# Performance work log

Hardware: AMD Instinct MI355X
Metric: run time of the kernel (lower is better)

Reference implementation:

```python
import jax, jax.numpy as jnp
import numpy as np

N_NODES = 100000
N_EDGES = 1600000
D_IN = 128
D_OUT = 128
BN_EPS = 1e-5


def setup_inputs() -> dict:
    key = jax.random.key(0)
    k1, k2, k3 = jax.random.split(key, 3)
    x = jax.random.normal(k1, (N_NODES, D_IN), dtype=jnp.float32)
    edge_index = jax.random.randint(k2, (2, N_EDGES), 0, N_NODES, dtype=jnp.int64)
    glorot = float(np.sqrt(6.0 / (D_IN + D_OUT)))
    W = jax.random.uniform(k3, (D_IN, D_OUT), dtype=jnp.float32, minval=-glorot, maxval=glorot)
    b = jnp.zeros((D_OUT,), dtype=jnp.float32)
    gamma = jnp.ones((D_OUT,), dtype=jnp.float32)
    beta = jnp.zeros((D_OUT,), dtype=jnp.float32)
    return {"x": x, "edge_index": edge_index, "W": W, "b": b, "gamma": gamma, "beta": beta}


def reference(x, edge_index, W, b, gamma, beta):
    N = x.shape[0]
    # Linear transform first (as in GCNConv.forward): [N, D_out]
    h = x @ W
    row, col = edge_index[0], edge_index[1]
    # remove_self_loops equivalent: zero out weights of self-loop edges (static shape)
    ew = (row != col).astype(h.dtype)
    loop = jnp.arange(N, dtype=edge_index.dtype)
    row_a = jnp.concatenate([row, loop])
    col_a = jnp.concatenate([col, loop])
    ew_a = jnp.concatenate([ew, jnp.ones((N,), h.dtype)])  # add_self_loops fill=1.0
    # D^{-1/2} A D^{-1/2}: degree over source (row) indices, as in GCNConv.norm
    deg = jax.ops.segment_sum(ew_a, row_a, num_segments=N)
    safe = jnp.where(deg > 0, deg, 1.0)
    deg_inv_sqrt = jnp.where(deg > 0, 1.0 / jnp.sqrt(safe), 0.0)
    norm = deg_inv_sqrt[row_a] * ew_a * deg_inv_sqrt[col_a]
    # message: norm * x_j (gather source), aggregate 'add' at target (col)
    msg = norm[:, None] * h[row_a]
    out = jax.ops.segment_sum(msg, col_a, num_segments=N) + b
    # activation
    out = jax.nn.relu(out)
    # BatchNorm1d (training mode: batch statistics, biased variance)
    mean = out.mean(axis=0)
    var = ((out - mean) ** 2).mean(axis=0)
    out = (out - mean) / jnp.sqrt(var + BN_EPS) * gamma + beta
    return out
```

## Files before the change

kernel.cpp:

```cpp
#include <hip/hip_runtime.h>
#include <math.h>

#define NN 100000
#define NE 1600000
#define D 128
#define BN_EPS 1e-5f
#define NCHUNK 391
#define GSZ4 25000
#define NCH 64
#define CH 25000
#define HW8 6250
#define HSTR 12500

typedef __attribute__((ext_vector_type(8))) short short8;
typedef __attribute__((ext_vector_type(4))) float f32x4;
typedef __attribute__((ext_vector_type(2))) float f32x2;


__device__ __forceinline__ unsigned bf_rne(float f) {
    unsigned u = __float_as_uint(f);
    return (u + 0x7fffu + ((u >> 16) & 1u)) >> 16;
}
__device__ __forceinline__ unsigned pk2(float lo, float hi) {
    return bf_rne(lo) | (bf_rne(hi) << 16);
}

__global__ __launch_bounds__(1024) void k_hist(const int* __restrict__ ei,
                                               unsigned* __restrict__ hist) {
    __shared__ unsigned loc[HSTR];
    const int g = blockIdx.x & 3;
    const int t = blockIdx.x >> 2;
    const int lo = g * GSZ4, hi = lo + GSZ4;
    for (int j = threadIdx.x; j < HSTR; j += 1024) loc[j] = 0u;
    __syncthreads();
    const int end = t * CH + CH;
    for (int i = t * CH + threadIdx.x; i < end; i += 1024) {
        int r = __builtin_nontemporal_load(ei + i);
        int c = __builtin_nontemporal_load(ei + NE + i);
        if (r != c) {
            if (c >= lo && c < hi) {
                int q = c - lo;
                atomicAdd(&loc[q >> 2], 1u << ((q & 3) << 3));
            }
            if (r >= lo && r < hi) {
                int q = r - lo;
                atomicAdd(&loc[HW8 + (q >> 2)], 1u << ((q & 3) << 3));
            }
        }
    }
    __syncthreads();
    unsigned* dst = hist + (unsigned)(g * NCH + t) * HSTR;
    for (int j = threadIdx.x; j < HSTR; j += 1024) dst[j] = loc[j];
}

__global__ void k_cvt(const float* __restrict__ x, unsigned* __restrict__ xh) {
    int i = blockIdx.x * blockDim.x + threadIdx.x;
    if (i < NN * 64) {
        f32x2 v = __builtin_nontemporal_load((const f32x2*)x + i);
        xh[i] = pk2(v.x, v.y);
    }
}

__global__ __launch_bounds__(256) void k_reduce(unsigned* __restrict__ hist,
                                                unsigned* __restrict__ cnt,
                                                float* __restrict__ dinv,
                                                const float* __restrict__ W,
                                                unsigned short* __restrict__ Wht) {
    int id = blockIdx.x * 256 + threadIdx.x;
    if (id < 4 * HW8) {
        int g = id / HW8;
        int w = id - g * HW8;
        unsigned base = (unsigned)(g * NCH) * HSTR + w;
        unsigned r0 = 0, r1 = 0, r2 = 0, r3 = 0;
        unsigned s0 = 0, s1 = 0, s2 = 0, s3 = 0;
        for (int t = 0; t < NCH; ++t) {
            unsigned idx = base + (unsigned)t * HSTR;
            unsigned v = hist[idx];
            hist[idx] = r0 | (r1 << 8) | (r2 << 16) | (r3 << 24);
            r0 += v & 255u; r1 += (v >> 8) & 255u;
            r2 += (v >> 16) & 255u; r3 += v >> 24;
            unsigned d = hist[idx + HW8];
            s0 += d & 255u; s1 += (d >> 8) & 255u;
            s2 += (d >> 16) & 255u; s3 += d >> 24;
        }
        int n0 = g * GSZ4 + 4 * w;
        cnt[n0]     = r0; cnt[n0 + 1] = r1; cnt[n0 + 2] = r2; cnt[n0 + 3] = r3;
        dinv[n0]     = rsqrtf((float)(s0 + 1u));
        dinv[n0 + 1] = rsqrtf((float)(s1 + 1u));
        dinv[n0 + 2] = rsqrtf((float)(s2 + 1u));
        dinv[n0 + 3] = rsqrtf((float)(s3 + 1u));
    } else {
        int i = id - 4 * HW8;
        if (i < D * D) {
            int k = i >> 7, c = i & 127;
            Wht[c * D + k] = (unsigned short)bf_rne(W[i]);
        }
    }
}

__global__ __launch_bounds__(256) void k_scan1(const unsigned* __restrict__ cnt,
                                               unsigned* __restrict__ part) {
    __shared__ unsigned s[256];
    int i = blockIdx.x * 256 + threadIdx.x;
    unsigned v = (i < NN) ? cnt[i] : 0u;
    s[threadIdx.x] = v;
    __syncthreads();
    for (int o = 128; o > 0; o >>= 1) {
        if (threadIdx.x < o) s[threadIdx.x] += s[threadIdx.x + o];
        __syncthreads();
    }
    if (threadIdx.x == 0) part[blockIdx.x] = s[0];
}

__global__ __launch_bounds__(512) void k_scan2(unsigned* __restrict__ part,
                                               float* __restrict__ sums8) {
    __shared__ unsigned s[512];
    int t = threadIdx.x;
    for (int j = t; j < 2048; j += 512) sums8[j] = 0.f;
    unsigned v = (t < NCHUNK) ? part[t] : 0u;
    s[t] = v;
    __syncthreads();
    for (int o = 1; o < 512; o <<= 1) {
        unsigned add = (t >= o) ? s[t - o] : 0u;
        __syncthreads();
        s[t] += add;
        __syncthreads();
    }
    if (t < NCHUNK) part[t] = s[t] - v;
}

__global__ __launch_bounds__(256) void k_scan3(const unsigned* __restrict__ cnt,
                                               const unsigned* __restrict__ part,
                                               unsigned* __restrict__ off) {
    __shared__ unsigned s[256];
    int i = blockIdx.x * 256 + threadIdx.x;
    int t = threadIdx.x;
    unsigned v = (i < NN) ? cnt[i] : 0u;
    s[t] = v;
    __syncthreads();
    for (int o = 1; o < 256; o <<= 1) {
        unsigned add = (t >= o) ? s[t - o] : 0u;
        __syncthreads();
        s[t] += add;
        __syncthreads();
    }
    if (i < NN) off[i] = part[blockIdx.x] + s[t] - v;
}

__global__ __launch_bounds__(1024) void k_scatter(const int* __restrict__ ei,
                                                  const unsigned* __restrict__ off,
                                                  const unsigned* __restrict__ hist,
                                                  int* __restrict__ esrc) {
    __shared__ unsigned curs[GSZ4 / 2];
    const int g = blockIdx.x & 3;
    const int t = blockIdx.x >> 2;
    const int lo = g * GSZ4, hi = lo + GSZ4;
    const unsigned* hb = hist + (unsigned)(g * NCH + t) * HSTR;
    for (int j = threadIdx.x; j < GSZ4 / 2; j += 1024) {
        unsigned hv = hb[j >> 1];
        unsigned sh = (j & 1) << 4;
        unsigned p0 = (hv >> sh) & 255u;
        unsigned p1 = (hv >> (sh + 8)) & 255u;
        curs[j] = p0 | (p1 << 16);
    }
    __syncthreads();
    const int end = t * CH + CH;
    for (int i = t * CH + threadIdx.x; i < end; i += 1024) {
        int r = __builtin_nontemporal_load(ei + i);
        int c = __builtin_nontemporal_load(ei + NE + i);
        if (r == c || c < lo || c >= hi) continue;
        int q = c - lo;
        unsigned sh = (q & 1) << 4;
        unsigned old = atomicAdd(&curs[q >> 1], 1u << sh);
        unsigned pos = off[c] + ((old >> sh) & 0xffffu);
        esrc[pos] = r;
    }
}

__global__ __launch_bounds__(256) void k_gather(const unsigned* __restrict__ xh,
                                                const float* __restrict__ dinv,
                                                const unsigned* __restrict__ off,
                                                const unsigned* __restrict__ cnt,
                                                const int* __restrict__ esrc,
                                                float* __restrict__ out) {
    const int lane = threadIdx.x & 63;
    const int wave = threadIdx.x >> 6;
    const int c = blockIdx.x * 4 + wave;
    if (c >= NN) return;

    const float dc = dinv[c];
    unsigned xc = xh[c * 64 + lane];
    float al = dc * __uint_as_float(xc << 16);
    float ah = dc * __uint_as_float(xc & 0xffff0000u);

    const int base = off[c];
    const int n = cnt[c];
    int i = 0;
    for (; i + 8 <= n; i += 8) {
        int   sv[8];
        float wv[8];
        unsigned pv[8];
        #pragma unroll
        for (int j = 0; j < 8; ++j) sv[j] = esrc[base + i + j];
        #pragma unroll
        for (int j = 0; j < 8; ++j) wv[j] = dinv[sv[j]];
        #pragma unroll
        for (int j = 0; j < 8; ++j) pv[j] = xh[sv[j] * 64 + lane];
        #pragma unroll
        for (int j = 0; j < 8; ++j) {
            al = fmaf(wv[j], __uint_as_float(pv[j] << 16), al);
            ah = fmaf(wv[j], __uint_as_float(pv[j] & 0xffff0000u), ah);
        }
    }
    for (; i + 4 <= n; i += 4) {
        int s0 = esrc[base + i], s1 = esrc[base + i + 1];
        int s2 = esrc[base + i + 2], s3 = esrc[base + i + 3];
        float w0 = dinv[s0], w1 = dinv[s1], w2 = dinv[s2], w3 = dinv[s3];
        unsigned p0 = xh[s0 * 64 + lane], p1 = xh[s1 * 64 + lane];
        unsigned p2 = xh[s2 * 64 + lane], p3 = xh[s3 * 64 + lane];
        al = fmaf(w0, __uint_as_float(p0 << 16), al);
        ah = fmaf(w0, __uint_as_float(p0 & 0xffff0000u), ah);
        al = fmaf(w1, __uint_as_float(p1 << 16), al);
        ah = fmaf(w1, __uint_as_float(p1 & 0xffff0000u), ah);
        al = fmaf(w2, __uint_as_float(p2 << 16), al);
        ah = fmaf(w2, __uint_as_float(p2 & 0xffff0000u), ah);
        al = fmaf(w3, __uint_as_float(p3 << 16), al);
        ah = fmaf(w3, __uint_as_float(p3 & 0xffff0000u), ah);
    }
    for (; i < n; ++i) {
        int s0 = esrc[base + i];
        float w0 = dinv[s0];
        unsigned p0 = xh[s0 * 64 + lane];
        al = fmaf(w0, __uint_as_float(p0 << 16), al);
        ah = fmaf(w0, __uint_as_float(p0 & 0xffff0000u), ah);
    }
    al *= dc;
    ah *= dc;
    *(float2*)&out[c * D + 2 * lane] = make_float2(al, ah);
}

__global__ __launch_bounds__(256, 1) void k_gemm(const float* __restrict__ out,
                                                 unsigned short* __restrict__ rh,
                                                 const unsigned short* __restrict__ Wht,
                                                 const float* __restrict__ b,
                                                 float* __restrict__ sums8) {
    __shared__ float sums_lds[256];
    const int lane = threadIdx.x & 63;
    const int wv = threadIdx.x >> 6;
    const int l15 = lane & 15, l4 = lane >> 4;

    if (threadIdx.x < 256) sums_lds[threadIdx.x] = 0.f;
    __syncthreads();

    short8 bfr[8][4];
    #pragma unroll
    for (int n = 0; n < 8; ++n)
        #pragma unroll
        for (int kk = 0; kk < 4; ++kk)
            bfr[n][kk] = *(const short8*)(Wht + (n * 16 + l15) * D + kk * 32 + l4 * 8);

    float bias8[8];
    #pragma unroll
    for (int n = 0; n < 8; ++n) bias8[n] = b[n * 16 + l15];

    float sl[8], s2l[8];
    #pragma unroll
    for (int n = 0; n < 8; ++n) { sl[n] = 0.f; s2l[n] = 0.f; }

    const int gw = blockIdx.x * 4 + wv;
    #pragma unroll
    for (int t = 0; t < 2; ++t) {
        const int tile = gw * 2 + t;
        if (tile < NN / 16) {
            const int row0 = tile * 16;
            short8 af[4];
            #pragma unroll
            for (int kk = 0; kk < 4; ++kk) {
                const float* ar = out + (row0 + l15) * D + kk * 32 + l4 * 8;
                float4 a0 = *(const float4*)ar;
                float4 a1 = *(const float4*)(ar + 4);
                union { short8 s; unsigned u[4]; } cv;
                cv.u[0] = pk2(a0.x, a0.y);
                cv.u[1] = pk2(a0.z, a0.w);
                cv.u[2] = pk2(a1.x, a1.y);
                cv.u[3] = pk2(a1.z, a1.w);
                af[kk] = cv.s;
            }
            f32x4 acc[8];
            #pragma unroll
            for (int n = 0; n < 8; ++n) acc[n] = (f32x4){0.f, 0.f, 0.f, 0.f};
            #pragma unroll
            for (int n = 0; n < 8; ++n)
                #pragma unroll
                for (int kk = 0; kk < 4; ++kk)
                    acc[n] = __builtin_amdgcn_mfma_f32_16x16x32_bf16(af[kk], bfr[n][kk],
                                                                     acc[n], 0, 0, 0);
            #pragma unroll
            for (int n = 0; n < 8; ++n)
                #pragma unroll
                for (int j = 0; j < 4; ++j) {
                    int row = row0 + l4 * 4 + j;
                    float v = fmaxf(acc[n][j] + bias8[n], 0.f);
                    rh[row * D + n * 16 + l15] = (unsigned short)bf_rne(v);
                    sl[n] += v;
                    s2l[n] = fmaf(v, v, s2l[n]);
                }
        }
    }

    #pragma unroll
    for (int n = 0; n < 8; ++n) {
        float a = sl[n], q = s2l[n];
        a += __shfl_xor(a, 16); a += __shfl_xor(a, 32);
        q += __shfl_xor(q, 16); q += __shfl_xor(q, 32);
        if (l4 == 0) {
            atomicAdd(&sums_lds[n * 16 + l15], a);
            atomicAdd(&sums_lds[128 + n * 16 + l15], q);
        }
    }
    __syncthreads();
    if (threadIdx.x < 256)
        unsafeAtomicAdd(&sums8[(blockIdx.x & 7) * 256 + threadIdx.x],
                        sums_lds[threadIdx.x]);
}

__global__ __launch_bounds__(256) void k_apply(const unsigned* __restrict__ rh,
                                               float* __restrict__ out,
                                               const float* __restrict__ gamma,
                                               const float* __restrict__ beta,
                                               const float* __restrict__ sums8) {
    const float invN = 1.f / (float)NN;
    const int tid = blockIdx.x * blockDim.x + threadIdx.x;
    const int stride = gridDim.x * blockDim.x;
    const int c4 = (tid & 31) * 4;

    float4 s4 = make_float4(0.f, 0.f, 0.f, 0.f);
    float4 q4 = make_float4(0.f, 0.f, 0.f, 0.f);
    #pragma unroll
    for (int k = 0; k < 8; ++k) {
        float4 a = *(const float4*)&sums8[k * 256 + c4];
        float4 q = *(const float4*)&sums8[k * 256 + 128 + c4];
        s4.x += a.x; s4.y += a.y; s4.z += a.z; s4.w += a.w;
        q4.x += q.x; q4.y += q.y; q4.z += q.z; q4.w += q.w;
    }
    float4 g4 = *(const float4*)&gamma[c4];
    float4 be = *(const float4*)&beta[c4];

    float mx = s4.x * invN, my = s4.y * invN, mz = s4.z * invN, mw = s4.w * invN;
    float scx = g4.x * rsqrtf(fmaxf(q4.x * invN - mx * mx, 0.f) + BN_EPS);
    float scy = g4.y * rsqrtf(fmaxf(q4.y * invN - my * my, 0.f) + BN_EPS);
    float scz = g4.z * rsqrtf(fmaxf(q4.z * invN - mz * mz, 0.f) + BN_EPS);
    float scw = g4.w * rsqrtf(fmaxf(q4.w * invN - mw * mw, 0.f) + BN_EPS);
    float shx = be.x - mx * scx, shy = be.y - my * scy;
    float shz = be.z - mz * scz, shw = be.w - mw * scw;

    for (int idx = tid; idx < NN * (D / 4); idx += stride) {
        const int row = idx >> 5;
        uint2 p = *(const uint2*)&rh[row * 64 + (tid & 31) * 2];
        float4 a;
        a.x = __uint_as_float(p.x << 16);
        a.y = __uint_as_float(p.x & 0xffff0000u);
        a.z = __uint_as_float(p.y << 16);
        a.w = __uint_as_float(p.y & 0xffff0000u);
        a.x = a.x * scx + shx;
        a.y = a.y * scy + shy;
        a.z = a.z * scz + shz;
        a.w = a.w * scw + shw;
        ((float4*)out)[idx] = a;
    }
}

extern "C" void kernel_launch(void* const* d_in, const int* in_sizes, int n_in,
                              void* d_out, int out_size, void* d_ws, size_t ws_size,
                              hipStream_t stream) {
    const float* x     = (const float*)d_in[0];
    const int*   ei    = (const int*)d_in[1];
    const float* W     = (const float*)d_in[2];
    const float* b     = (const float*)d_in[3];
    const float* gamma = (const float*)d_in[4];
    const float* beta  = (const float*)d_in[5];
    float*       out   = (float*)d_out;

    char* ws = (char*)d_ws;
    float*          dinv  = (float*)ws;
    unsigned*       cnt   = (unsigned*)(ws + 400000);
    unsigned*       off   = (unsigned*)(ws + 800000);
    unsigned*       part  = (unsigned*)(ws + 1200000);
    float*          sums8 = (float*)(ws + 1202048);
    int*            esrc  = (int*)(ws + 1210368);
    unsigned*       hist  = (unsigned*)(ws + 7610368);
    unsigned*       xh    = (unsigned*)(ws + 20410368);
    unsigned short* Wht   = (unsigned short*)(ws + 46010368);

    k_hist<<<NCH * 4, 1024, 0, stream>>>(ei, hist);
    k_cvt<<<25000, 256, 0, stream>>>(x, xh);
    k_reduce<<<(4 * HW8 + D * D + 255) / 256, 256, 0, stream>>>(hist, cnt, dinv, W, Wht);
    k_scan1<<<NCHUNK, 256, 0, stream>>>(cnt, part);
    k_scan2<<<1, 512, 0, stream>>>(part, sums8);
    k_scan3<<<NCHUNK, 256, 0, stream>>>(cnt, part, off);
    k_scatter<<<NCH * 4, 1024, 0, stream>>>(ei, off, hist, esrc);
    k_gather<<<25000, 256, 0, stream>>>(xh, dinv, off, cnt, esrc, out);
    k_gemm<<<782, 256, 0, stream>>>(out, (unsigned short*)xh, Wht, b, sums8);
    k_apply<<<2048, 256, 0, stream>>>(xh, out, gamma, beta, sums8);
}
```

Baseline: 227.8 us.

## Store aggregated features as bf16, fuse scan1 into reduce, vectorize cvt and scan3

Measured after the change: 212.0 us. 1.07x faster.

```diff
diff --git a/kernel.cpp b/kernel.cpp
--- a/kernel.cpp
+++ b/kernel.cpp
@@ -5,16 +5,15 @@
 #define NE 1600000
 #define D 128
 #define BN_EPS 1e-5f
-#define NCHUNK 391
 #define GSZ4 25000
 #define NCH 64
 #define CH 25000
 #define HW8 6250
 #define HSTR 12500
+#define NPART 98
 
 typedef __attribute__((ext_vector_type(8))) short short8;
 typedef __attribute__((ext_vector_type(4))) float f32x4;
-typedef __attribute__((ext_vector_type(2))) float f32x2;
 
 
 __device__ __forceinline__ unsigned bf_rne(float f) {
@@ -55,9 +54,12 @@
 
 __global__ void k_cvt(const float* __restrict__ x, unsigned* __restrict__ xh) {
     int i = blockIdx.x * blockDim.x + threadIdx.x;
-    if (i < NN * 64) {
-        f32x2 v = __builtin_nontemporal_load((const f32x2*)x + i);
-        xh[i] = pk2(v.x, v.y);
+    if (i < NN * 32) {
+        f32x4 v = __builtin_nontemporal_load((const f32x4*)x + i);
+        uint2 o;
+        o.x = pk2(v.x, v.y);
+        o.y = pk2(v.z, v.w);
+        ((uint2*)xh)[i] = o;
     }
 }
 
@@ -65,8 +67,11 @@
                                                 unsigned* __restrict__ cnt,
                                                 float* __restrict__ dinv,
                                                 const float* __restrict__ W,
-                                                unsigned short* __restrict__ Wht) {
+                                                unsigned short* __restrict__ Wht,
+                                                unsigned* __restrict__ part) {
+    __shared__ unsigned ps[256];
     int id = blockIdx.x * 256 + threadIdx.x;
+    unsigned mysum = 0;
     if (id < 4 * HW8) {
         int g = id / HW8;
         int w = id - g * HW8;
@@ -83,12 +88,13 @@
             s0 += d & 255u; s1 += (d >> 8) & 255u;
             s2 += (d >> 16) & 255u; s3 += d >> 24;
         }
-        int n0 = g * GSZ4 + 4 * w;
+        int n0 = 4 * id;
         cnt[n0]     = r0; cnt[n0 + 1] = r1; cnt[n0 + 2] = r2; cnt[n0 + 3] = r3;
         dinv[n0]     = rsqrtf((float)(s0 + 1u));
         dinv[n0 + 1] = rsqrtf((float)(s1 + 1u));
         dinv[n0 + 2] = rsqrtf((float)(s2 + 1u));
         dinv[n0 + 3] = rsqrtf((float)(s3 + 1u));
+        mysum = r0 + r1 + r2 + r3;
     } else {
         int i = id - 4 * HW8;
         if (i < D * D) {
@@ -96,20 +102,15 @@
             Wht[c * D + k] = (unsigned short)bf_rne(W[i]);
         }
     }
-}
-
-__global__ __launch_bounds__(256) void k_scan1(const unsigned* __restrict__ cnt,
-                                               unsigned* __restrict__ part) {
-    __shared__ unsigned s[256];
-    int i = blockIdx.x * 256 + threadIdx.x;
-    unsigned v = (i < NN) ? cnt[i] : 0u;
-    s[threadIdx.x] = v;
-    __syncthreads();
-    for (int o = 128; o > 0; o >>= 1) {
-        if (threadIdx.x < o) s[threadIdx.x] += s[threadIdx.x + o];
+    if (blockIdx.x < NPART) {
+        ps[threadIdx.x] = mysum;
         __syncthreads();
-    }
-    if (threadIdx.x == 0) part[blockIdx.x] = s[0];
+        for (int o = 128; o > 0; o >>= 1) {
+            if (threadIdx.x < o) ps[threadIdx.x] += ps[threadIdx.x + o];
+            __syncthreads();
+        }
+        if (threadIdx.x == 0) part[blockIdx.x] = ps[0];
+    }
 }
 
 __global__ __launch_bounds__(512) void k_scan2(unsigned* __restrict__ part,
@@ -117,7 +118,7 @@
     __shared__ unsigned s[512];
     int t = threadIdx.x;
     for (int j = t; j < 2048; j += 512) sums8[j] = 0.f;
-    unsigned v = (t < NCHUNK) ? part[t] : 0u;
+    unsigned v = (t < NPART) ? part[t] : 0u;
     s[t] = v;
     __syncthreads();
     for (int o = 1; o < 512; o <<= 1) {
@@ -126,17 +127,26 @@
         s[t] += add;
         __syncthreads();
     }
-    if (t < NCHUNK) part[t] = s[t] - v;
+    if (t < NPART) part[t] = s[t] - v;
 }
 
 __global__ __launch_bounds__(256) void k_scan3(const unsigned* __restrict__ cnt,
                                                const unsigned* __restrict__ part,
                                                unsigned* __restrict__ off) {
     __shared__ unsigned s[256];
-    int i = blockIdx.x * 256 + threadIdx.x;
-    int t = threadIdx.x;
-    unsigned v = (i < NN) ? cnt[i] : 0u;
-    s[t] = v;
+    const int t = threadIdx.x;
+    const int n0 = (blockIdx.x * 256 + t) * 4;
+    unsigned c0 = 0, c1 = 0, c2 = 0, c3 = 0;
+    if (n0 + 3 < NN) {
+        uint4 v = *(const uint4*)&cnt[n0];
+        c0 = v.x; c1 = v.y; c2 = v.z; c3 = v.w;
+    } else if (n0 < NN) {
+        c0 = cnt[n0];
+        if (n0 + 1 < NN) c1 = cnt[n0 + 1];
+        if (n0 + 2 < NN) c2 = cnt[n0 + 2];
+    }
+    unsigned mysum = c0 + c1 + c2 + c3;
+    s[t] = mysum;
     __syncthreads();
     for (int o = 1; o < 256; o <<= 1) {
         unsigned add = (t >= o) ? s[t - o] : 0u;
@@ -144,7 +154,13 @@
         s[t] += add;
         __syncthreads();
     }
-    if (i < NN) off[i] = part[blockIdx.x] + s[t] - v;
+    unsigned e = part[blockIdx.x] + s[t] - mysum;
+    if (n0 < NN) {
+        off[n0] = e;
+        if (n0 + 1 < NN) off[n0 + 1] = e + c0;
+        if (n0 + 2 < NN) off[n0 + 2] = e + c0 + c1;
+        if (n0 + 3 < NN) off[n0 + 3] = e + c0 + c1 + c2;
+    }
 }
 
 __global__ __launch_bounds__(1024) void k_scatter(const int* __restrict__ ei,
@@ -182,7 +198,7 @@
                                                 const unsigned* __restrict__ off,
                                                 const unsigned* __restrict__ cnt,
                                                 const int* __restrict__ esrc,
-                                                float* __restrict__ out) {
+                                                unsigned* __restrict__ outh) {
     const int lane = threadIdx.x & 63;
     const int wave = threadIdx.x >> 6;
     const int c = blockIdx.x * 4 + wave;
@@ -234,12 +250,10 @@
         al = fmaf(w0, __uint_as_float(p0 << 16), al);
         ah = fmaf(w0, __uint_as_float(p0 & 0xffff0000u), ah);
     }
-    al *= dc;
-    ah *= dc;
-    *(float2*)&out[c * D + 2 * lane] = make_float2(al, ah);
-}
-
-__global__ __launch_bounds__(256, 1) void k_gemm(const float* __restrict__ out,
+    outh[c * 64 + lane] = pk2(al * dc, ah * dc);
+}
+
+__global__ __launch_bounds__(256, 1) void k_gemm(const unsigned short* __restrict__ aggh,
                                                  unsigned short* __restrict__ rh,
                                                  const unsigned short* __restrict__ Wht,
                                                  const float* __restrict__ b,
@@ -275,17 +289,8 @@
             const int row0 = tile * 16;
             short8 af[4];
             #pragma unroll
-            for (int kk = 0; kk < 4; ++kk) {
-                const float* ar = out + (row0 + l15) * D + kk * 32 + l4 * 8;
-                float4 a0 = *(const float4*)ar;
-                float4 a1 = *(const float4*)(ar + 4);
-                union { short8 s; unsigned u[4]; } cv;
-                cv.u[0] = pk2(a0.x, a0.y);
-                cv.u[1] = pk2(a0.z, a0.w);
-                cv.u[2] = pk2(a1.x, a1.y);
-                cv.u[3] = pk2(a1.z, a1.w);
-                af[kk] = cv.s;
-            }
+            for (int kk = 0; kk < 4; ++kk)
+                af[kk] = *(const short8*)(aggh + (row0 + l15) * D + kk * 32 + l4 * 8);
             f32x4 acc[8];
             #pragma unroll
             for (int n = 0; n < 8; ++n) acc[n] = (f32x4){0.f, 0.f, 0.f, 0.f};
@@ -393,13 +398,12 @@
     unsigned short* Wht   = (unsigned short*)(ws + 46010368);
 
     k_hist<<<NCH * 4, 1024, 0, stream>>>(ei, hist);
-    k_cvt<<<25000, 256, 0, stream>>>(x, xh);
-    k_reduce<<<(4 * HW8 + D * D + 255) / 256, 256, 0, stream>>>(hist, cnt, dinv, W, Wht);
-    k_scan1<<<NCHUNK, 256, 0, stream>>>(cnt, part);
+    k_cvt<<<(NN * 32 + 255) / 256, 256, 0, stream>>>(x, xh);
+    k_reduce<<<(4 * HW8 + D * D + 255) / 256, 256, 0, stream>>>(hist, cnt, dinv, W, Wht, part);
     k_scan2<<<1, 512, 0, stream>>>(part, sums8);
-    k_scan3<<<NCHUNK, 256, 0, stream>>>(cnt, part, off);
+    k_scan3<<<NPART, 256, 0, stream>>>(cnt, part, off);
     k_scatter<<<NCH * 4, 1024, 0, stream>>>(ei, off, hist, esrc);
-    k_gather<<<25000, 256, 0, stream>>>(xh, dinv, off, cnt, esrc, out);
-    k_gemm<<<782, 256, 0, stream>>>(out, (unsigned short*)xh, Wht, b, sums8);
+    k_gather<<<25000, 256, 0, stream>>>(xh, dinv, off, cnt, esrc, (unsigned*)out);
+    k_gemm<<<782, 256, 0, stream>>>((const unsigned short*)out, (unsigned short*)xh, Wht, b, sums8);
     k_apply<<<2048, 256, 0, stream>>>(xh, out, gamma, beta, sums8);
 }
```
